# Optimization experiments

Hardware: AMD Instinct MI355X
Metric: run time of the kernel (lower is better)

Reference implementation:

```python
import jax, jax.numpy as jnp
import numpy as np

KSIZE = 3
PAD = (KSIZE - 1) // 2
SIG = 0.3 * ((KSIZE - 1) * 0.5 - 1) + 0.8  # sigma_space == sigma_density == 0.8
INV2S2 = 1.0 / (2.0 * SIG * SIG)


def _gauss_space():
    c = KSIZE // 2
    xs = np.arange(KSIZE, dtype=np.float32)
    gx, gy = np.meshgrid(xs, xs, indexing='xy')
    w = np.exp(-(((gx - c) ** 2 + (gy - c) ** 2)) * INV2S2)
    w = w / w.sum()
    return jnp.asarray(w, dtype=jnp.float32)


def _patches(x):
    # x: [N,C,H,W] -> [N,C,H,W,k,k], zero padding (matches F.pad value=0)
    H, W = x.shape[-2], x.shape[-1]
    xp = jnp.pad(x, ((0, 0), (0, 0), (PAD, PAD), (PAD, PAD)))
    rows = []
    for i in range(KSIZE):
        cols = [xp[:, :, i:i + H, j:j + W] for j in range(KSIZE)]
        rows.append(jnp.stack(cols, axis=-1))
    return jnp.stack(rows, axis=-2)


def setup_inputs() -> dict:
    key = jax.random.key(0)
    k1, k2, k3 = jax.random.split(key, 3)
    B, V, C, H, W = 2, 4, 3, 512, 512
    depth = jax.random.uniform(k1, (B, V, 1, H, W), dtype=jnp.float32)
    color = jax.random.uniform(k2, (B, V, C, H, W), dtype=jnp.float32)
    mask = jax.random.uniform(k3, (B, V, 1, H, W), dtype=jnp.float32)
    return {"depth": depth, "color": color, "mask": mask}


def reference(depth, color, mask):
    B, V, C, H, W = color.shape
    d = depth.reshape(B * V, 1, H, W)
    m = mask.reshape(B * V, 1, H, W)
    c = color.reshape(B * V, C, H, W)

    dp = _patches(d)  # [N,1,H,W,k,k]
    cp = _patches(c)  # [N,C,H,W,k,k]
    mp = _patches(m)  # [N,1,H,W,k,k]

    # depth (density) gaussian weight, normalized per-pixel over the window
    wd = jnp.exp(-((dp - d[..., None, None]) ** 2) * INV2S2)
    wd = wd / wd.sum(axis=(-1, -2), keepdims=True)

    # color gaussian weight summed over channels, normalized per-pixel
    wc = jnp.exp(-((cp - c[..., None, None]) ** 2) * INV2S2).sum(axis=1, keepdims=True)
    wc = wc / wc.sum(axis=(-1, -2), keepdims=True)

    ws = _gauss_space().reshape(1, 1, 1, 1, KSIZE, KSIZE)

    w = wd * wc * ws * mp + 1e-7  # [N,1,H,W,k,k]
    out = (w * cp).sum(axis=(-1, -2)) / w.sum(axis=(-1, -2))  # [N,C,H,W]
    return out.reshape(B, V, C, H, W)
```

## Files before the change

### kernel.cpp

```cpp
#include <hip/hip_runtime.h>


constexpr int HH = 512;
constexpr int WW = 512;
constexpr int HW = HH * WW;

#define KEXP (-1.1271055f)
#define E2(x) __builtin_amdgcn_exp2f(x)
#define WS0f 0.2724967f
#define WS1f 0.1247577f
#define WS2f 0.0571180f

__global__ __launch_bounds__(256) void bilateral_v6(
    const float* __restrict__ depth,
    const float* __restrict__ color,
    const float* __restrict__ mask,
    float* __restrict__ out)
{
    const int lane = threadIdx.x & 63;
    const int b    = blockIdx.x;
    const int logical = (b & 7) * 128 + (b >> 3);
    const int wg   = logical * 4 + (int)(threadIdx.x >> 6);
    const int n    = wg >> 9;
    const int rem  = wg & 511;
    const int hp   = rem >> 1;
    const int half = rem & 1;
    const int rA   = hp * 2;
    const int c0   = half * 256 + lane * 4;

    const float* dptr = depth + (size_t)n * HW;
    const float* mptr = mask  + (size_t)n * HW;
    const float* xptr = color + (size_t)n * 3 * HW;
    const float* yptr = xptr + HW;
    const float* zptr = xptr + 2 * HW;

    const bool hasL = (c0 > 0);
    const bool hasR = (c0 < WW - 4);

    float AD[6], AM[6], AX[6], AY[6], AZ[6];
    float BD[6], BM[6], BX[6], BY[6], BZ[6];
    float PD[6], PM[6], PX[6], PY[6], PZ[6];

#define LOADP(W, base, ro) do {                                              \
    const float4 _q = *reinterpret_cast<const float4*>((base) + (ro));       \
    W[1] = _q.x; W[2] = _q.y; W[3] = _q.z; W[4] = _q.w;                      \
    W[0] = hasL ? (base)[(ro) - 1] : 0.0f;                                   \
    W[5] = hasR ? (base)[(ro) + 4] : 0.0f;                                   \
} while (0)

#define LOADW(D_, M_, X_, Y_, Z_, r) do {                                    \
    const int _ro = (r) * WW + c0;                                           \
    LOADP(D_, dptr, _ro); LOADP(M_, mptr, _ro);                              \
    LOADP(X_, xptr, _ro); LOADP(Y_, yptr, _ro); LOADP(Z_, zptr, _ro);        \
} while (0)

    float aSwd[4], aSwc[4], aSt[4], aS0[4], aS1[4], aS2[4];
    float bSwd[4], bSwc[4], bSt[4], bS0[4], bS1[4], bS2[4];
    #pragma unroll
    for (int i = 0; i < 4; ++i) {
        aSwd[i]=0.f; aSwc[i]=0.f; aSt[i]=0.f; aS0[i]=0.f; aS1[i]=0.f; aS2[i]=0.f;
        bSwd[i]=0.f; bSwc[i]=0.f; bSt[i]=0.f; bS0[i]=0.f; bS1[i]=0.f; bS2[i]=0.f;
    }

#define HPASS(D_, M_, X_, Y_, Z_, Swd, Swc, St, S0, S1, S2) do {             \
    float hwd[5], hwc[5];                                                    \
    _Pragma("unroll") for (int j = 0; j < 5; ++j) {                          \
        const float dd = D_[j] - D_[j + 1];                                  \
        hwd[j] = E2(KEXP * dd * dd);                                         \
        const float f0 = X_[j] - X_[j + 1];                                  \
        const float f1 = Y_[j] - Y_[j + 1];                                  \
        const float f2 = Z_[j] - Z_[j + 1];                                  \
        hwc[j] = E2(KEXP * f0 * f0) + E2(KEXP * f1 * f1)                     \
               + E2(KEXP * f2 * f2);                                         \
    }                                                                        \
    _Pragma("unroll") for (int i = 0; i < 4; ++i) {                          \
        const int ci = i + 1;                                                \
        { const float t = (3.0f * WS0f) * M_[ci];      \
          Swd[i] += 1.0f; Swc[i] += 3.0f; St[i] += t;                        \
          S0[i] += t * X_[ci]; S1[i] += t * Y_[ci]; S2[i] += t * Z_[ci]; }   \
        { const float t = hwd[i] * hwc[i] * WS1f * M_[i];          \
          Swd[i] += hwd[i]; Swc[i] += hwc[i]; St[i] += t;                    \
          S0[i] += t * X_[i]; S1[i] += t * Y_[i]; S2[i] += t * Z_[i]; }      \
        { const float t = hwd[i+1] * hwc[i+1] * WS1f * M_[i+2];    \
          Swd[i] += hwd[i+1]; Swc[i] += hwc[i+1]; St[i] += t;                \
          S0[i] += t * X_[i+2]; S1[i] += t * Y_[i+2]; S2[i] += t * Z_[i+2];} \
    }                                                                        \
} while (0)

#define SIDE(TD, TM, TX, TY, TZ, RD, RX, RY, RZ, Swd, Swc, St, S0, S1, S2) do { \
    _Pragma("unroll") for (int i = 0; i < 4; ++i) {                          \
        const float cd = RD[i + 1];                                          \
        const float cx = RX[i + 1];                                          \
        const float cy = RY[i + 1];                                          \
        const float cz = RZ[i + 1];                                          \
        _Pragma("unroll") for (int dj = 0; dj < 3; ++dj) {                   \
            const int c = i + dj;                                            \
            const float dd = TD[c] - cd;                                     \
            const float wd = E2(KEXP * dd * dd);                             \
            const float f0 = TX[c] - cx;                                     \
            const float f1 = TY[c] - cy;                                     \
            const float f2 = TZ[c] - cz;                                     \
            const float wc = E2(KEXP * f0 * f0) + E2(KEXP * f1 * f1)         \
                           + E2(KEXP * f2 * f2);                             \
            const float ws = (dj == 1) ? WS1f : WS2f;                        \
            const float t = wd * wc * ws * TM[c];                            \
            Swd[i] += wd; Swc[i] += wc; St[i] += t;                          \
            S0[i] += t * TX[c]; S1[i] += t * TY[c]; S2[i] += t * TZ[c];      \
        }                                                                    \
    }                                                                        \
} while (0)

    const bool hasUp = (hp > 0);
    const bool hasDn = (hp < 255);

    LOADW(AD, AM, AX, AY, AZ, rA);
    LOADW(BD, BM, BX, BY, BZ, rA + 1);
    if (hasUp) LOADW(PD, PM, PX, PY, PZ, rA - 1);

    HPASS(AD, AM, AX, AY, AZ, aSwd, aSwc, aSt, aS0, aS1, aS2);
    HPASS(BD, BM, BX, BY, BZ, bSwd, bSwc, bSt, bS0, bS1, bS2);

    if (hasUp) {
        SIDE(PD, PM, PX, PY, PZ, AD, AX, AY, AZ,
             aSwd, aSwc, aSt, aS0, aS1, aS2);
    }

    if (hasDn) LOADW(PD, PM, PX, PY, PZ, rA + 2);

    #pragma unroll
    for (int a = 0; a < 6; ++a) {
        #pragma unroll
        for (int db = -1; db <= 1; ++db) {
            const int bb = a + db;
            if (bb < 0 || bb > 5) continue;
            const bool useA = (a >= 1 && a <= 4);
            const bool useB = (bb >= 1 && bb <= 4);
            if (!useA && !useB) continue;
            const float dd = AD[a] - BD[bb];
            const float pwd = E2(KEXP * dd * dd);
            const float f0 = AX[a] - BX[bb];
            const float f1 = AY[a] - BY[bb];
            const float f2 = AZ[a] - BZ[bb];
            const float pwc = E2(KEXP * f0 * f0) + E2(KEXP * f1 * f1)
                            + E2(KEXP * f2 * f2);
            const float g = pwd * pwc;
            const float ws = (db == 0) ? WS1f : WS2f;
            if (useA) {
                const int i = a - 1;
                const float t = g * ws * BM[bb];
                aSwd[i] += pwd; aSwc[i] += pwc; aSt[i] += t;
                aS0[i] += t * BX[bb]; aS1[i] += t * BY[bb]; aS2[i] += t * BZ[bb];
            }
            if (useB) {
                const int i = bb - 1;
                const float t = g * ws * AM[a];
                bSwd[i] += pwd; bSwc[i] += pwc; bSt[i] += t;
                bS0[i] += t * AX[a]; bS1[i] += t * AY[a]; bS2[i] += t * AZ[a];
            }
        }
    }

    if (hasDn) {
        SIDE(PD, PM, PX, PY, PZ, BD, BX, BY, BZ,
             bSwd, bSwc, bSt, bS0, bS1, bS2);
    }

    float oa0[4], oa1[4], oa2[4], ob0[4], ob1[4], ob2[4];
    #pragma unroll
    for (int i = 0; i < 4; ++i) {
        const float invA = __builtin_amdgcn_rcpf(aSt[i] + 9e-7f * aSwd[i] * aSwc[i]);
        oa0[i] = aS0[i] * invA; oa1[i] = aS1[i] * invA; oa2[i] = aS2[i] * invA;
        const float invB = __builtin_amdgcn_rcpf(bSt[i] + 9e-7f * bSwd[i] * bSwc[i]);
        ob0[i] = bS0[i] * invB; ob1[i] = bS1[i] * invB; ob2[i] = bS2[i] * invB;
    }

    float* po = out + (size_t)n * 3 * HW + rA * WW + c0;
    *reinterpret_cast<float4*>(po)               = make_float4(oa0[0], oa0[1], oa0[2], oa0[3]);
    *reinterpret_cast<float4*>(po + HW)          = make_float4(oa1[0], oa1[1], oa1[2], oa1[3]);
    *reinterpret_cast<float4*>(po + 2 * HW)      = make_float4(oa2[0], oa2[1], oa2[2], oa2[3]);
    *reinterpret_cast<float4*>(po + WW)          = make_float4(ob0[0], ob0[1], ob0[2], ob0[3]);
    *reinterpret_cast<float4*>(po + WW + HW)     = make_float4(ob1[0], ob1[1], ob1[2], ob1[3]);
    *reinterpret_cast<float4*>(po + WW + 2 * HW) = make_float4(ob2[0], ob2[1], ob2[2], ob2[3]);
}

extern "C" void kernel_launch(void* const* d_in, const int* in_sizes, int n_in,
                              void* d_out, int out_size, void* d_ws, size_t ws_size,
                              hipStream_t stream) {
    const float* depth = (const float*)d_in[0];
    const float* color = (const float*)d_in[1];
    const float* mask  = (const float*)d_in[2];
    float* out = (float*)d_out;

    bilateral_v6<<<1024, 256, 0, stream>>>(depth, color, mask, out);
}
```

Measured before the change: 27.36 us.

## Stage 34x72 halo tiles of all planes in LDS before the bilateral filter

Each block now cooperatively loads a 32x64 output tile plus a one-row, four-column halo for depth, mask and the three colour planes into shared memory with float4 global reads. Threads then read their 6-wide windows from LDS instead of issuing redundant, misaligned scalar global loads for neighbour rows and columns. Borders are handled by zero-filling the halo, which removes the per-thread edge branches. The cost is about 48KB of LDS per block and a barrier that serialises loading and compute. The launch-bounds hint of 3 blocks per CU may also limit occupancy.

```diff
diff --git a/kernel.cpp b/kernel.cpp
--- a/kernel.cpp
+++ b/kernel.cpp
@@ -1,9 +1,12 @@
 #include <hip/hip_runtime.h>
 
 
-constexpr int HH = 512;
-constexpr int WW = 512;
-constexpr int HW = HH * WW;
+constexpr int HH = 512, WW = 512, HW = HH * WW;
+constexpr int TR = 32, TC = 64;
+constexpr int LR = TR + 2;
+constexpr int LC = TC + 8;
+constexpr int PL = LR * LC;
+constexpr int NGRP = LR * (LC / 4);
 
 #define KEXP (-1.1271055f)
 #define E2(x) __builtin_amdgcn_exp2f(x)
@@ -11,22 +14,21 @@
 #define WS1f 0.1247577f
 #define WS2f 0.0571180f
 
-__global__ __launch_bounds__(256) void bilateral_v6(
+__global__ __launch_bounds__(256, 3) void bilateral_v7(
     const float* __restrict__ depth,
     const float* __restrict__ color,
     const float* __restrict__ mask,
     float* __restrict__ out)
 {
-    const int lane = threadIdx.x & 63;
-    const int b    = blockIdx.x;
-    const int logical = (b & 7) * 128 + (b >> 3);
-    const int wg   = logical * 4 + (int)(threadIdx.x >> 6);
-    const int n    = wg >> 9;
-    const int rem  = wg & 511;
-    const int hp   = rem >> 1;
-    const int half = rem & 1;
-    const int rA   = hp * 2;
-    const int c0   = half * 256 + lane * 4;
+    __shared__ __align__(16) float lds[5 * PL];
+
+    const int tid = threadIdx.x;
+    const int b   = blockIdx.x;
+    const int n   = b >> 7;
+    const int rg  = (b >> 3) & 15;
+    const int cg  = b & 7;
+    const int rb  = rg * TR;
+    const int cb  = cg * TC;
 
     const float* dptr = depth + (size_t)n * HW;
     const float* mptr = mask  + (size_t)n * HW;
@@ -34,24 +36,51 @@
     const float* yptr = xptr + HW;
     const float* zptr = xptr + 2 * HW;
 
-    const bool hasL = (c0 > 0);
-    const bool hasR = (c0 < WW - 4);
+    {
+        const float* planes[5] = { dptr, mptr, xptr, yptr, zptr };
+        #pragma unroll
+        for (int p = 0; p < 5; ++p) {
+            const float* src = planes[p];
+            #pragma unroll
+            for (int k = 0; k < 3; ++k) {
+                const int f = tid + k * 256;
+                if (f < NGRP) {
+                    const int row = f / 18;
+                    const int grp = f - row * 18;
+                    const int gr  = rb - 1 + row;
+                    const int gc  = cb - 4 + grp * 4;
+                    float4 v = make_float4(0.f, 0.f, 0.f, 0.f);
+                    if (((unsigned)gr < (unsigned)HH) &&
+                        ((unsigned)gc < (unsigned)WW))
+                        v = *reinterpret_cast<const float4*>(src + gr * WW + gc);
+                    *reinterpret_cast<float4*>(&lds[p * PL + f * 4]) = v;
+                }
+            }
+        }
+    }
+    __syncthreads();
+
+    const int rp = tid >> 4;
+    const int c4 = tid & 15;
+    const int lc = c4 * 4;
+    const int lr = rp * 2;
 
     float AD[6], AM[6], AX[6], AY[6], AZ[6];
     float BD[6], BM[6], BX[6], BY[6], BZ[6];
-    float PD[6], PM[6], PX[6], PY[6], PZ[6];
-
-#define LOADP(W, base, ro) do {                                              \
-    const float4 _q = *reinterpret_cast<const float4*>((base) + (ro));       \
-    W[1] = _q.x; W[2] = _q.y; W[3] = _q.z; W[4] = _q.w;                      \
-    W[0] = hasL ? (base)[(ro) - 1] : 0.0f;                                   \
-    W[5] = hasR ? (base)[(ro) + 4] : 0.0f;                                   \
-} while (0)
-
-#define LOADW(D_, M_, X_, Y_, Z_, r) do {                                    \
-    const int _ro = (r) * WW + c0;                                           \
-    LOADP(D_, dptr, _ro); LOADP(M_, mptr, _ro);                              \
-    LOADP(X_, xptr, _ro); LOADP(Y_, yptr, _ro); LOADP(Z_, zptr, _ro);        \
+    float TD[6], TM[6], TX[6], TY[6], TZ[6];
+
+#define RDW(W, p, row) do {                                                  \
+    const float* _b = &lds[(p) * PL + (row) * LC + lc];                      \
+    const float2 _e0 = *reinterpret_cast<const float2*>(_b + 2);             \
+    const float4 _m  = *reinterpret_cast<const float4*>(_b + 4);             \
+    const float2 _e1 = *reinterpret_cast<const float2*>(_b + 8);             \
+    W[0] = _e0.y; W[1] = _m.x; W[2] = _m.y; W[3] = _m.z; W[4] = _m.w;        \
+    W[5] = _e1.x;                                                            \
+} while (0)
+
+#define RDROW(D_, M_, X_, Y_, Z_, row) do {                                  \
+    RDW(D_, 0, row); RDW(M_, 1, row); RDW(X_, 2, row);                       \
+    RDW(Y_, 3, row); RDW(Z_, 4, row);                                        \
 } while (0)
 
     float aSwd[4], aSwc[4], aSt[4], aS0[4], aS1[4], aS2[4];
@@ -75,19 +104,19 @@
     }                                                                        \
     _Pragma("unroll") for (int i = 0; i < 4; ++i) {                          \
         const int ci = i + 1;                                                \
-        { const float t = (3.0f * WS0f) * M_[ci];      \
+        { const float t = (3.0f * WS0f) * M_[ci];                            \
           Swd[i] += 1.0f; Swc[i] += 3.0f; St[i] += t;                        \
           S0[i] += t * X_[ci]; S1[i] += t * Y_[ci]; S2[i] += t * Z_[ci]; }   \
-        { const float t = hwd[i] * hwc[i] * WS1f * M_[i];          \
+        { const float t = hwd[i] * hwc[i] * WS1f * M_[i];                    \
           Swd[i] += hwd[i]; Swc[i] += hwc[i]; St[i] += t;                    \
           S0[i] += t * X_[i]; S1[i] += t * Y_[i]; S2[i] += t * Z_[i]; }      \
-        { const float t = hwd[i+1] * hwc[i+1] * WS1f * M_[i+2];    \
+        { const float t = hwd[i+1] * hwc[i+1] * WS1f * M_[i+2];              \
           Swd[i] += hwd[i+1]; Swc[i] += hwc[i+1]; St[i] += t;                \
           S0[i] += t * X_[i+2]; S1[i] += t * Y_[i+2]; S2[i] += t * Z_[i+2];} \
     }                                                                        \
 } while (0)
 
-#define SIDE(TD, TM, TX, TY, TZ, RD, RX, RY, RZ, Swd, Swc, St, S0, S1, S2) do { \
+#define SIDE(D_, M_, X_, Y_, Z_, RD, RX, RY, RZ, Swd, Swc, St, S0, S1, S2) do { \
     _Pragma("unroll") for (int i = 0; i < 4; ++i) {                          \
         const float cd = RD[i + 1];                                          \
         const float cx = RX[i + 1];                                          \
@@ -95,37 +124,32 @@
         const float cz = RZ[i + 1];                                          \
         _Pragma("unroll") for (int dj = 0; dj < 3; ++dj) {                   \
             const int c = i + dj;                                            \
-            const float dd = TD[c] - cd;                                     \
+            const float dd = D_[c] - cd;                                     \
             const float wd = E2(KEXP * dd * dd);                             \
-            const float f0 = TX[c] - cx;                                     \
-            const float f1 = TY[c] - cy;                                     \
-            const float f2 = TZ[c] - cz;                                     \
+            const float f0 = X_[c] - cx;                                     \
+            const float f1 = Y_[c] - cy;                                     \
+            const float f2 = Z_[c] - cz;                                     \
             const float wc = E2(KEXP * f0 * f0) + E2(KEXP * f1 * f1)         \
                            + E2(KEXP * f2 * f2);                             \
             const float ws = (dj == 1) ? WS1f : WS2f;                        \
-            const float t = wd * wc * ws * TM[c];                            \
+            const float t = wd * wc * ws * M_[c];                            \
             Swd[i] += wd; Swc[i] += wc; St[i] += t;                          \
-            S0[i] += t * TX[c]; S1[i] += t * TY[c]; S2[i] += t * TZ[c];      \
+            S0[i] += t * X_[c]; S1[i] += t * Y_[c]; S2[i] += t * Z_[c];      \
         }                                                                    \
     }                                                                        \
 } while (0)
 
-    const bool hasUp = (hp > 0);
-    const bool hasDn = (hp < 255);
-
-    LOADW(AD, AM, AX, AY, AZ, rA);
-    LOADW(BD, BM, BX, BY, BZ, rA + 1);
-    if (hasUp) LOADW(PD, PM, PX, PY, PZ, rA - 1);
+    RDROW(AD, AM, AX, AY, AZ, lr + 1);
+    RDROW(BD, BM, BX, BY, BZ, lr + 2);
+    RDROW(TD, TM, TX, TY, TZ, lr);
 
     HPASS(AD, AM, AX, AY, AZ, aSwd, aSwc, aSt, aS0, aS1, aS2);
     HPASS(BD, BM, BX, BY, BZ, bSwd, bSwc, bSt, bS0, bS1, bS2);
 
-    if (hasUp) {
-        SIDE(PD, PM, PX, PY, PZ, AD, AX, AY, AZ,
-             aSwd, aSwc, aSt, aS0, aS1, aS2);
-    }
-
-    if (hasDn) LOADW(PD, PM, PX, PY, PZ, rA + 2);
+    SIDE(TD, TM, TX, TY, TZ, AD, AX, AY, AZ,
+         aSwd, aSwc, aSt, aS0, aS1, aS2);
+
+    RDROW(TD, TM, TX, TY, TZ, lr + 3);
 
     #pragma unroll
     for (int a = 0; a < 6; ++a) {
@@ -160,10 +184,8 @@
         }
     }
 
-    if (hasDn) {
-        SIDE(PD, PM, PX, PY, PZ, BD, BX, BY, BZ,
-             bSwd, bSwc, bSt, bS0, bS1, bS2);
-    }
+    SIDE(TD, TM, TX, TY, TZ, BD, BX, BY, BZ,
+         bSwd, bSwc, bSt, bS0, bS1, bS2);
 
     float oa0[4], oa1[4], oa2[4], ob0[4], ob1[4], ob2[4];
     #pragma unroll
@@ -174,7 +196,9 @@
         ob0[i] = bS0[i] * invB; ob1[i] = bS1[i] * invB; ob2[i] = bS2[i] * invB;
     }
 
-    float* po = out + (size_t)n * 3 * HW + rA * WW + c0;
+    const int orow = rb + rp * 2;
+    const int ocol = cb + lc;
+    float* po = out + (size_t)n * 3 * HW + orow * WW + ocol;
     *reinterpret_cast<float4*>(po)               = make_float4(oa0[0], oa0[1], oa0[2], oa0[3]);
     *reinterpret_cast<float4*>(po + HW)          = make_float4(oa1[0], oa1[1], oa1[2], oa1[3]);
     *reinterpret_cast<float4*>(po + 2 * HW)      = make_float4(oa2[0], oa2[1], oa2[2], oa2[3]);
@@ -191,5 +215,5 @@
     const float* mask  = (const float*)d_in[2];
     float* out = (float*)d_out;
 
-    bilateral_v6<<<1024, 256, 0, stream>>>(depth, color, mask, out);
+    bilateral_v7<<<1024, 256, 0, stream>>>(depth, color, mask, out);
 }
```

New measurement: 33.69 us. 23.1% more time.
